# Kernel tuning notes

Hardware: AMD Instinct MI355X
Metric: run time of the kernel (lower is better)

## Reference

```python
import jax, jax.numpy as jnp
import numpy as np

IN_FEATURES = 1024
OUT_FEATURES = 1024
GRID_SIZE = 5
SPLINE_ORDER = 3
GRID_RANGE = (-1.0, 1.0)


def make_grid():
    h = (GRID_RANGE[1] - GRID_RANGE[0]) / GRID_SIZE
    g = jnp.arange(-SPLINE_ORDER, GRID_SIZE + SPLINE_ORDER + 1, dtype=jnp.float32) * h + GRID_RANGE[0]
    return jnp.tile(g[None, :], (IN_FEATURES, 1))  # (in, G + 2k + 1)


def b_splines(x, grid):
    # x: (N, in), grid: (in, G+2k+1) -> bases: (N, in, G+k)
    xe = x[..., None]
    bases = ((xe >= grid[:, :-1]) & (xe < grid[:, 1:])).astype(x.dtype)
    for k in range(1, SPLINE_ORDER + 1):
        left = (xe - grid[:, :-(k + 1)]) / (grid[:, k:-1] - grid[:, :-(k + 1)])
        right = (grid[:, k + 1:] - xe) / (grid[:, k + 1:] - grid[:, 1:-k])
        bases = left * bases[:, :, :-1] + right * bases[:, :, 1:]
    return bases


def setup_inputs() -> dict:
    key = jax.random.key(0)
    k1, k2, k3 = jax.random.split(key, 3)
    x = jax.random.uniform(k1, (8192, IN_FEATURES), dtype=jnp.float32)
    # lecun_normal-style init: std = 1/sqrt(fan_in)
    base_weight = jax.random.normal(k2, (OUT_FEATURES, IN_FEATURES), dtype=jnp.float32) / np.sqrt(IN_FEATURES)
    coeff = GRID_SIZE + SPLINE_ORDER
    spline_weight = jax.random.normal(k3, (OUT_FEATURES, IN_FEATURES, coeff), dtype=jnp.float32) / np.sqrt(IN_FEATURES * coeff)
    spline_scaler = jnp.ones((OUT_FEATURES, IN_FEATURES), dtype=jnp.float32)
    grid = make_grid()
    return {"x": x, "grid": grid, "base_weight": base_weight,
            "spline_weight": spline_weight, "spline_scaler": spline_scaler}


def reference(x, grid, base_weight, spline_weight, spline_scaler):
    N = x.shape[0]
    base_out = jax.nn.silu(x) @ base_weight.T  # (N, out)
    bases = b_splines(x, grid)                 # (N, in, G+k)
    scaled_sw = spline_weight * spline_scaler[..., None]  # (out, in, G+k)
    spline_out = bases.reshape(N, -1) @ scaled_sw.reshape(OUT_FEATURES, -1).T  # (N, out)
    return base_out + spline_out
```

## Files before the change

kernel.cpp:

```cpp
#include <hip/hip_runtime.h>
#include <hip/hip_bf16.h>

#define IN_F 1024
#define OUT_F 1024
#define KTOT (IN_F * 9)
#define M_ROWS 8192

#define BM 256
#define BN 128
#define BK 64
#define NT (KTOT / BK)

#define A_TILE_E 16384
#define B_TILE_E 8192

typedef short bf16x8 __attribute__((ext_vector_type(8)));
typedef int   i32x4  __attribute__((ext_vector_type(4)));
typedef float f32x4  __attribute__((ext_vector_type(4)));

#define AS1 __attribute__((address_space(1)))
#define AS3 __attribute__((address_space(3)))

__device__ __forceinline__ void kan_basis_fast(
    float xv, const float* __restrict__ g,
    const float* __restrict__ inv1, const float* __restrict__ inv2,
    const float* __restrict__ inv3, float* __restrict__ out) {
  float b[11];
#pragma unroll
  for (int j = 0; j < 11; ++j)
    b[j] = (xv >= g[j] && xv < g[j + 1]) ? 1.0f : 0.0f;
#pragma unroll
  for (int j = 0; j < 10; ++j)
    b[j] = (xv - g[j]) * inv1[j] * b[j] + (g[j + 2] - xv) * inv1[j + 1] * b[j + 1];
#pragma unroll
  for (int j = 0; j < 9; ++j)
    b[j] = (xv - g[j]) * inv2[j] * b[j] + (g[j + 3] - xv) * inv2[j + 1] * b[j + 1];
#pragma unroll
  for (int j = 0; j < 8; ++j)
    b[j] = (xv - g[j]) * inv3[j] * b[j] + (g[j + 4] - xv) * inv3[j + 1] * b[j + 1];
#pragma unroll
  for (int j = 0; j < 8; ++j) out[j] = b[j];
}

__global__ __launch_bounds__(256) void expand_a(
    const float* __restrict__ x, const float* __restrict__ grid,
    __hip_bfloat16* __restrict__ A, int row0, int nrows) {
  const int tid = threadIdx.x;
  const int lane = tid & 63;
  const int wvx = tid >> 6;
  const int l15 = lane & 15;
  const int lhi = lane >> 4;

  const int nb = blockIdx.x >> 3;
  const int ib = blockIdx.x & 7;
  const int n_l = nb * 16 + l15;
  const int i0 = ib * 128 + wvx * 32 + lhi * 8;

  const int bm = n_l >> 8, wm = (n_l >> 6) & 3, m = (n_l >> 4) & 3;

  float g[12];
  const float* gp = grid + (size_t)i0 * 12;
#pragma unroll
  for (int j = 0; j < 12; ++j) g[j] = gp[j];
  float inv1[11], inv2[10], inv3[9];
#pragma unroll
  for (int j = 0; j < 11; ++j) inv1[j] = 1.0f / (g[j + 1] - g[j]);
#pragma unroll
  for (int j = 0; j < 10; ++j) inv2[j] = 1.0f / (g[j + 2] - g[j]);
#pragma unroll
  for (int j = 0; j < 9; ++j)  inv3[j] = 1.0f / (g[j + 3] - g[j]);

  const float* xp = x + (size_t)(row0 + n_l) * IN_F + i0;
  float xs[8];
  *(f32x4*)&xs[0] = *(const f32x4*)xp;
  *(f32x4*)&xs[4] = *(const f32x4*)(xp + 4);

  bf16x8 out[9];
#pragma unroll
  for (int j = 0; j < 8; ++j) {
    float xv = xs[j];
    float bas[8];
    kan_basis_fast(xv, g, inv1, inv2, inv3, bas);
    float s = xv / (1.0f + __expf(-xv));
    out[0][j] = (short)__bfloat16_as_ushort(__float2bfloat16(s));
#pragma unroll
    for (int c = 0; c < 8; ++c)
      out[c + 1][j] = (short)__bfloat16_as_ushort(__float2bfloat16(bas[c]));
  }

#pragma unroll
  for (int c = 0; c < 9; ++c) {
    int k0 = c * IN_F + i0;
    int kt = k0 >> 6;
    int kk = (k0 >> 5) & 1;
    size_t frag = ((((size_t)bm * NT + kt) * 4 + wm) * 4 + m) * 2 + kk;
    *(bf16x8*)(A + frag * 512 + lane * 8) = out[c];
  }
}

__global__ __launch_bounds__(256) void pack_b(
    const float* __restrict__ bw, const float* __restrict__ sw,
    const float* __restrict__ sc, __hip_bfloat16* __restrict__ B) {
  const int tid = threadIdx.x;
  const int lane = tid & 63;
  const int wid = blockIdx.x * 4 + (tid >> 6);
  const int og = wid >> 5;
  const int ib32 = wid & 31;
  const int bn = og >> 3, colg = og & 7;
  const int l15 = lane & 15, lhi = lane >> 4;
  const int o = og * 16 + l15;
  const int i0 = ib32 * 32 + lhi * 8;

  float bwv[8], scv[8];
  const float* bp = bw + (size_t)o * IN_F + i0;
  const float* sp = sc + (size_t)o * IN_F + i0;
  *(f32x4*)&bwv[0] = *(const f32x4*)bp;
  *(f32x4*)&bwv[4] = *(const f32x4*)(bp + 4);
  *(f32x4*)&scv[0] = *(const f32x4*)sp;
  *(f32x4*)&scv[4] = *(const f32x4*)(sp + 4);

  bf16x8 out[9];
#pragma unroll
  for (int j = 0; j < 8; ++j) {
    out[0][j] = (short)__bfloat16_as_ushort(__float2bfloat16(bwv[j]));
    const float* swp = sw + ((size_t)o * IN_F + i0 + j) * 8;
    float swv[8];
    *(f32x4*)&swv[0] = *(const f32x4*)swp;
    *(f32x4*)&swv[4] = *(const f32x4*)(swp + 4);
#pragma unroll
    for (int c = 0; c < 8; ++c)
      out[c + 1][j] = (short)__bfloat16_as_ushort(__float2bfloat16(swv[c] * scv[j]));
  }

#pragma unroll
  for (int c = 0; c < 9; ++c) {
    int kt = c * 16 + (ib32 >> 1);
    int kk = ib32 & 1;
    size_t frag = ((size_t)bn * NT + kt) * 16 + colg * 2 + kk;
    *(bf16x8*)(B + frag * 512 + lane * 8) = out[c];
  }
}


__device__ __forceinline__ void gld16(const __hip_bfloat16* g, __hip_bfloat16* l) {
  __builtin_amdgcn_global_load_lds((AS1 void*)g, (AS3 void*)l, 16, 0, 0);
}

__device__ __forceinline__ bf16x8 dsr128(uint32_t addr) {
  i32x4 r;
  asm volatile("ds_read_b128 %0, %1" : "=v"(r) : "v"(addr));
  return __builtin_bit_cast(bf16x8, r);
}

#define SB __builtin_amdgcn_sched_barrier(0)

#define SLOT_B 49152
#define SLOT_E 24576

#define READ_FRAGS(dA, dB, slot, h) do {                                   \
    uint32_t s_ = ldsB + (uint32_t)(slot) * SLOT_B;                        \
    _Pragma("unroll")                                                      \
    for (int m_ = 0; m_ < 4; ++m_) dA[m_] = dsr128(s_ + aOff[h][m_]);      \
    _Pragma("unroll")                                                      \
    for (int n_ = 0; n_ < 4; ++n_) dB[n_] = dsr128(s_ + bOff[h][n_]);      \
  } while (0)

#define MFMA_BURST(sA, sB) do {                                            \
    __builtin_amdgcn_s_setprio(1);                                         \
    _Pragma("unroll")                                                      \
    for (int m_ = 0; m_ < 4; ++m_)                                         \
      _Pragma("unroll")                                                    \
      for (int n_ = 0; n_ < 4; ++n_)                                       \
        acc[m_][n_] = __builtin_amdgcn_mfma_f32_16x16x32_bf16(             \
            sA[m_], sB[n_], acc[m_][n_], 0, 0, 0);                         \
    __builtin_amdgcn_s_setprio(0);                                         \
  } while (0)

#define STAGE_T(slot, t) do {                                              \
    __hip_bfloat16* d_ = ldsP + (slot) * SLOT_E;                           \
    const __hip_bfloat16* aT_ = aG + (size_t)(t) * A_TILE_E;               \
    const __hip_bfloat16* bT_ = bG + (size_t)(t) * B_TILE_E;               \
    gld16(aT_,         d_ + dstE);                                         \
    gld16(aT_ + 4096,  d_ + dstE + 4096);                                  \
    gld16(aT_ + 8192,  d_ + dstE + 8192);                                  \
    gld16(aT_ + 12288, d_ + dstE + 12288);                                 \
    gld16(bT_,         d_ + 16384 + dstE);                                 \
    gld16(bT_ + 4096,  d_ + 16384 + dstE + 4096);                          \
  } while (0)

#define TILE_FULL(t) do {                                                  \
    const int nxt_ = cur == 2 ? 0 : cur + 1;                               \
    const int stg_ = cur == 0 ? 2 : cur - 1;                               \
    READ_FRAGS(ga, gb, cur, 1);                               \
    STAGE_T(stg_, (t) + 2);                                  \
    SB;                                                                    \
    asm volatile("s_waitcnt lgkmcnt(8)" ::: "memory"); SB;                 \
    MFMA_BURST(fa, fb);                                                    \
    SB;                                                                    \
    asm volatile("s_waitcnt lgkmcnt(0)" ::: "memory"); SB;                 \
    asm volatile("s_waitcnt vmcnt(6)" ::: "memory"); SB;                   \
    __builtin_amdgcn_s_barrier(); SB;                     \
    READ_FRAGS(fa, fb, nxt_, 0);                               \
    SB;                                                                    \
    MFMA_BURST(ga, gb);                                                    \
    SB;                                                                    \
    cur = nxt_;                                                            \
  } while (0)

#define TILE_NT2() do {                                                    \
    const int nxt_ = cur == 2 ? 0 : cur + 1;                               \
    READ_FRAGS(ga, gb, cur, 1);                                            \
    SB;                                                                    \
    asm volatile("s_waitcnt lgkmcnt(8)" ::: "memory"); SB;                 \
    MFMA_BURST(fa, fb);                                                    \
    SB;                                                                    \
    asm volatile("s_waitcnt lgkmcnt(0)" ::: "memory"); SB;                 \
    asm volatile("s_waitcnt vmcnt(0)" ::: "memory"); SB;                   \
    __builtin_amdgcn_s_barrier(); SB;                                      \
    READ_FRAGS(fa, fb, nxt_, 0);                                           \
    SB;                                                                    \
    MFMA_BURST(ga, gb);                                                    \
    SB;                                                                    \
    cur = nxt_;                                                            \
  } while (0)

#define TILE_LAST() do {                                                   \
    READ_FRAGS(ga, gb, cur, 1);                                            \
    SB;                                                                    \
    asm volatile("s_waitcnt lgkmcnt(8)" ::: "memory"); SB;                 \
    MFMA_BURST(fa, fb);                                                    \
    SB;                                                                    \
    asm volatile("s_waitcnt lgkmcnt(0)" ::: "memory"); SB;                 \
    MFMA_BURST(ga, gb);                                                    \
    SB;                                                                    \
  } while (0)

__global__ __launch_bounds__(512, 2) void gemm_v11(
    const __hip_bfloat16* __restrict__ A, const __hip_bfloat16* __restrict__ B,
    float* __restrict__ C) {
  __shared__ __align__(16) __hip_bfloat16 S[3][SLOT_E];

  const int nwg = gridDim.x;
  const int q = nwg >> 3;
  const int L = (blockIdx.x & 7) * q + (blockIdx.x >> 3);
  const int bm = L >> 3, bn = L & 7;

  const int tid = threadIdx.x;
  const int lane = tid & 63;
  const int wv = tid >> 6;
  const int wm = wv >> 1;
  const int wn = wv & 1;
  const int l15 = lane & 15, lhi = lane >> 4;

  const __hip_bfloat16* aG = A + (size_t)bm * NT * A_TILE_E + (wv * 64 + lane) * 8;
  const __hip_bfloat16* bG = B + (size_t)bn * NT * B_TILE_E + (wv * 64 + lane) * 8;
  __hip_bfloat16* ldsP = &S[0][0];
  const int dstE = wv * 512;

  const uint32_t ldsB = (uint32_t)(uintptr_t)(AS3 const void*)&S[0][0];
  uint32_t aOff[2][4], bOff[2][4];
#pragma unroll
  for (int h = 0; h < 2; ++h)
#pragma unroll
    for (int m = 0; m < 4; ++m) {
      aOff[h][m] = (uint32_t)((wm * 8 + m * 2 + h) * 1024 + lane * 16);
      bOff[h][m] = (uint32_t)(32768 + ((wn * 4 + m) * 2 + h) * 1024 + lane * 16);
    }

  f32x4 acc[4][4];
#pragma unroll
  for (int m = 0; m < 4; ++m)
#pragma unroll
    for (int n = 0; n < 4; ++n) acc[m][n] = f32x4{0.f, 0.f, 0.f, 0.f};

  bf16x8 fa[4], fb[4];
  bf16x8 ga[4], gb[4];

  STAGE_T(0, 0);
  STAGE_T(1, 1);
  asm volatile("s_waitcnt vmcnt(6)" ::: "memory");
  SB;
  __builtin_amdgcn_s_barrier();
  SB;
  READ_FRAGS(fa, fb, 0, 0);
  SB;

  int cur = 0;
  for (int t = 0; t < NT - 2; ++t) TILE_FULL(t);
  TILE_NT2();
  TILE_LAST();

#pragma unroll
  for (int m = 0; m < 4; ++m)
#pragma unroll
    for (int n = 0; n < 4; ++n) {
      int col = bn * BN + wn * 64 + n * 16 + l15;
      int row0 = bm * BM + wm * 64 + m * 16 + lhi * 4;
#pragma unroll
      for (int j = 0; j < 4; ++j)
        C[(size_t)(row0 + j) * OUT_F + col] = acc[m][n][j];
    }
}

__global__ __launch_bounds__(256) void kan_naive(
    const float* __restrict__ x, const float* __restrict__ grid,
    const float* __restrict__ bw, const float* __restrict__ sw,
    const float* __restrict__ sc, float* __restrict__ out) {
  __shared__ float s_act[IN_F];
  __shared__ float s_bas[IN_F * 8];
  int n = blockIdx.x;
  for (int i = threadIdx.x; i < IN_F; i += 256) {
    float xv = x[(size_t)n * IN_F + i];
    float g[12];
    const float* gp = grid + i * 12;
#pragma unroll
    for (int t = 0; t < 12; ++t) g[t] = gp[t];
    float b[11];
#pragma unroll
    for (int j = 0; j < 11; ++j)
      b[j] = (xv >= g[j] && xv < g[j + 1]) ? 1.0f : 0.0f;
#pragma unroll
    for (int k = 1; k <= 3; ++k)
#pragma unroll
      for (int j = 0; j < 11 - k; ++j) {
        float left = (xv - g[j]) / (g[j + k] - g[j]);
        float right = (g[j + k + 1] - xv) / (g[j + k + 1] - g[j + 1]);
        b[j] = left * b[j] + right * b[j + 1];
      }
    s_act[i] = xv / (1.0f + __expf(-xv));
#pragma unroll
    for (int c = 0; c < 8; ++c) s_bas[i * 8 + c] = b[c];
  }
  __syncthreads();
  for (int o = threadIdx.x; o < OUT_F; o += 256) {
    float acc = 0.f;
    const float* bwo = bw + (size_t)o * IN_F;
    const float* swo = sw + (size_t)o * IN_F * 8;
    const float* sco = sc + (size_t)o * IN_F;
    for (int i = 0; i < IN_F; ++i) {
      acc += s_act[i] * bwo[i];
      float p = 0.f;
#pragma unroll
      for (int c = 0; c < 8; ++c) p += s_bas[i * 8 + c] * swo[i * 8 + c];
      acc += p * sco[i];
    }
    out[(size_t)n * OUT_F + o] = acc;
  }
}

extern "C" void kernel_launch(void* const* d_in, const int* in_sizes, int n_in,
                              void* d_out, int out_size, void* d_ws, size_t ws_size,
                              hipStream_t stream) {
  const float* x  = (const float*)d_in[0];
  const float* grid = (const float*)d_in[1];
  const float* bw = (const float*)d_in[2];
  const float* sw = (const float*)d_in[3];
  const float* sc = (const float*)d_in[4];
  float* out = (float*)d_out;

  const size_t Bbytes = (size_t)OUT_F * KTOT * 2;
  const size_t rowBytes = (size_t)KTOT * 2;

  if (ws_size >= Bbytes + 256 * rowBytes) {
    __hip_bfloat16* Bp = (__hip_bfloat16*)d_ws;
    __hip_bfloat16* Ap = (__hip_bfloat16*)((char*)d_ws + Bbytes);
    size_t arows = (ws_size - Bbytes) / rowBytes;
    int chunk = (int)((arows / 256) * 256);
    if (chunk > M_ROWS) chunk = M_ROWS;

    pack_b<<<OUT_F * 128 / 256, 256, 0, stream>>>(bw, sw, sc, Bp);
    for (int r0 = 0; r0 < M_ROWS; r0 += chunk) {
      int rows = M_ROWS - r0 < chunk ? M_ROWS - r0 : chunk;
      expand_a<<<(rows / 16) * 8, 256, 0, stream>>>(x, grid, Ap, r0, rows);
      gemm_v11<<<(rows / BM) * 8, 512, 0, stream>>>(Ap, Bp, out + (size_t)r0 * OUT_F);
    }
  } else {
    kan_naive<<<M_ROWS, 256, 0, stream>>>(x, grid, bw, sw, sc, out);
  }
}
```

Baseline: 183.4 us.

## Use 256x256 tiles with split-K halves and atomic accumulation in GEMM

Enlarges each workgroup's output tile from 256x128 to 256x256 and splits the K dimension into two halves across workgroups, with results summed via atomicAdd into a zero-initialised output. Staging moves from a triple buffer to a double buffer, and LDS reads now use immediate offsets, which cuts address arithmetic. The aim is higher arithmetic intensity per loaded byte while keeping the same workgroup count. The cost is an extra memset, atomic traffic on the output, nondeterministic summation order, and higher register pressure from 32 accumulators per wave.

```diff
diff --git a/kernel.cpp b/kernel.cpp
--- a/kernel.cpp
+++ b/kernel.cpp
@@ -6,10 +6,9 @@
 #define KTOT (IN_F * 9)
 #define M_ROWS 8192
 
-#define BM 256
-#define BN 128
 #define BK 64
 #define NT (KTOT / BK)
+#define NT_H (NT / 2)
 
 #define A_TILE_E 16384
 #define B_TILE_E 8192
@@ -106,7 +105,7 @@
   const int wid = blockIdx.x * 4 + (tid >> 6);
   const int og = wid >> 5;
   const int ib32 = wid & 31;
-  const int bn = og >> 3, colg = og & 7;
+  const int obn = og >> 3, colg = og & 7;
   const int l15 = lane & 15, lhi = lane >> 4;
   const int o = og * 16 + l15;
   const int i0 = ib32 * 32 + lhi * 8;
@@ -136,7 +135,7 @@
   for (int c = 0; c < 9; ++c) {
     int kt = c * 16 + (ib32 >> 1);
     int kk = ib32 & 1;
-    size_t frag = ((size_t)bn * NT + kt) * 16 + colg * 2 + kk;
+    size_t frag = ((size_t)obn * NT + kt) * 16 + colg * 2 + kk;
     *(bf16x8*)(B + frag * 512 + lane * 8) = out[c];
   }
 }
@@ -146,29 +145,39 @@
   __builtin_amdgcn_global_load_lds((AS1 void*)g, (AS3 void*)l, 16, 0, 0);
 }
 
-__device__ __forceinline__ bf16x8 dsr128(uint32_t addr) {
-  i32x4 r;
-  asm volatile("ds_read_b128 %0, %1" : "=v"(r) : "v"(addr));
-  return __builtin_bit_cast(bf16x8, r);
-}
+#define DSRO(dst, addr, IMM)                                               \
+  asm volatile("ds_read_b128 %0, %1 offset:" #IMM : "=v"(dst) : "v"(addr))
 
 #define SB __builtin_amdgcn_sched_barrier(0)
 
-#define SLOT_B 49152
-#define SLOT_E 24576
-
-#define READ_FRAGS(dA, dB, slot, h) do {                                   \
-    uint32_t s_ = ldsB + (uint32_t)(slot) * SLOT_B;                        \
-    _Pragma("unroll")                                                      \
-    for (int m_ = 0; m_ < 4; ++m_) dA[m_] = dsr128(s_ + aOff[h][m_]);      \
-    _Pragma("unroll")                                                      \
-    for (int n_ = 0; n_ < 4; ++n_) dB[n_] = dsr128(s_ + bOff[h][n_]);      \
-  } while (0)
-
-#define MFMA_BURST(sA, sB) do {                                            \
+#define SLOT_E 32768
+#define SLOT_B 65536
+
+#define READ_A_KK0(d, aA) do {                                             \
+    DSRO(d[0], aA, 0);     DSRO(d[1], aA, 2048);                           \
+    DSRO(d[2], aA, 4096);  DSRO(d[3], aA, 6144);                           \
+    DSRO(d[4], aA, 8192);  DSRO(d[5], aA, 10240);                          \
+    DSRO(d[6], aA, 12288); DSRO(d[7], aA, 14336);                          \
+  } while (0)
+#define READ_A_KK1(d, aA) do {                                             \
+    DSRO(d[0], aA, 1024);  DSRO(d[1], aA, 3072);                           \
+    DSRO(d[2], aA, 5120);  DSRO(d[3], aA, 7168);                           \
+    DSRO(d[4], aA, 9216);  DSRO(d[5], aA, 11264);                          \
+    DSRO(d[6], aA, 13312); DSRO(d[7], aA, 15360);                          \
+  } while (0)
+#define READ_B_KK0(d, bA) do {                                             \
+    DSRO(d[0], bA, 0);     DSRO(d[1], bA, 2048);                           \
+    DSRO(d[2], bA, 4096);  DSRO(d[3], bA, 6144);                           \
+  } while (0)
+#define READ_B_KK1(d, bA) do {                                             \
+    DSRO(d[0], bA, 1024);  DSRO(d[1], bA, 3072);                           \
+    DSRO(d[2], bA, 5120);  DSRO(d[3], bA, 7168);                           \
+  } while (0)
+
+#define MFMA_B(sA, sB) do {                                                \
     __builtin_amdgcn_s_setprio(1);                                         \
     _Pragma("unroll")                                                      \
-    for (int m_ = 0; m_ < 4; ++m_)                                         \
+    for (int m_ = 0; m_ < 8; ++m_)                                         \
       _Pragma("unroll")                                                    \
       for (int n_ = 0; n_ < 4; ++n_)                                       \
         acc[m_][n_] = __builtin_amdgcn_mfma_f32_16x16x32_bf16(             \
@@ -176,129 +185,105 @@
     __builtin_amdgcn_s_setprio(0);                                         \
   } while (0)
 
-#define STAGE_T(slot, t) do {                                              \
-    __hip_bfloat16* d_ = ldsP + (slot) * SLOT_E;                           \
-    const __hip_bfloat16* aT_ = aG + (size_t)(t) * A_TILE_E;               \
-    const __hip_bfloat16* bT_ = bG + (size_t)(t) * B_TILE_E;               \
-    gld16(aT_,         d_ + dstE);                                         \
-    gld16(aT_ + 4096,  d_ + dstE + 4096);                                  \
-    gld16(aT_ + 8192,  d_ + dstE + 8192);                                  \
-    gld16(aT_ + 12288, d_ + dstE + 12288);                                 \
-    gld16(bT_,         d_ + 16384 + dstE);                                 \
-    gld16(bT_ + 4096,  d_ + 16384 + dstE + 4096);                          \
-  } while (0)
-
-#define TILE_FULL(t) do {                                                  \
-    const int nxt_ = cur == 2 ? 0 : cur + 1;                               \
-    const int stg_ = cur == 0 ? 2 : cur - 1;                               \
-    READ_FRAGS(ga, gb, cur, 1);                               \
-    STAGE_T(stg_, (t) + 2);                                  \
+#define STAGE12(DST) do {                                                  \
+    gld16(aGp,          (DST) + dstE);                                     \
+    gld16(aGp + 4096,   (DST) + dstE + 4096);                              \
+    gld16(aGp + 8192,   (DST) + dstE + 8192);                              \
+    gld16(aGp + 12288,  (DST) + dstE + 12288);                             \
+    gld16(bGp0,         (DST) + dstE + 16384);                             \
+    gld16(bGp0 + 4096,  (DST) + dstE + 20480);                             \
+    gld16(bGp1,         (DST) + dstE + 24576);                             \
+    gld16(bGp1 + 4096,  (DST) + dstE + 28672);                             \
+    aGp += 16384; bGp0 += 8192; bGp1 += 8192;                              \
+  } while (0)
+
+#define TILE_V12(cA, cB, nA, nB, STAGE_, READN_) do {                      \
+    READ_A_KK1(ga, cA); READ_B_KK1(gb, cB);                   \
+    STAGE_                                                                 \
     SB;                                                                    \
-    asm volatile("s_waitcnt lgkmcnt(8)" ::: "memory"); SB;                 \
-    MFMA_BURST(fa, fb);                                                    \
-    SB;                                                                    \
-    asm volatile("s_waitcnt lgkmcnt(0)" ::: "memory"); SB;                 \
-    asm volatile("s_waitcnt vmcnt(6)" ::: "memory"); SB;                   \
-    __builtin_amdgcn_s_barrier(); SB;                     \
-    READ_FRAGS(fa, fb, nxt_, 0);                               \
-    SB;                                                                    \
-    MFMA_BURST(ga, gb);                                                    \
-    SB;                                                                    \
-    cur = nxt_;                                                            \
-  } while (0)
-
-#define TILE_NT2() do {                                                    \
-    const int nxt_ = cur == 2 ? 0 : cur + 1;                               \
-    READ_FRAGS(ga, gb, cur, 1);                                            \
-    SB;                                                                    \
-    asm volatile("s_waitcnt lgkmcnt(8)" ::: "memory"); SB;                 \
-    MFMA_BURST(fa, fb);                                                    \
+    asm volatile("s_waitcnt lgkmcnt(12)" ::: "memory"); SB;                \
+    MFMA_B(fa, fb);                                                        \
     SB;                                                                    \
     asm volatile("s_waitcnt lgkmcnt(0)" ::: "memory"); SB;                 \
     asm volatile("s_waitcnt vmcnt(0)" ::: "memory"); SB;                   \
-    __builtin_amdgcn_s_barrier(); SB;                                      \
-    READ_FRAGS(fa, fb, nxt_, 0);                                           \
+    __builtin_amdgcn_s_barrier(); SB;               \
+    READN_                                                                 \
     SB;                                                                    \
-    MFMA_BURST(ga, gb);                                                    \
+    MFMA_B(ga, gb);                                                        \
     SB;                                                                    \
-    cur = nxt_;                                                            \
-  } while (0)
-
-#define TILE_LAST() do {                                                   \
-    READ_FRAGS(ga, gb, cur, 1);                                            \
-    SB;                                                                    \
-    asm volatile("s_waitcnt lgkmcnt(8)" ::: "memory"); SB;                 \
-    MFMA_BURST(fa, fb);                                                    \
-    SB;                                                                    \
-    asm volatile("s_waitcnt lgkmcnt(0)" ::: "memory"); SB;                 \
-    MFMA_BURST(ga, gb);                                                    \
-    SB;                                                                    \
-  } while (0)
-
-__global__ __launch_bounds__(512, 2) void gemm_v11(
+  } while (0)
+
+#define READN12(nA, nB) READ_A_KK0(fa, nA); READ_B_KK0(fb, nB);
+
+__global__ __launch_bounds__(512, 2) void gemm_v12(
     const __hip_bfloat16* __restrict__ A, const __hip_bfloat16* __restrict__ B,
     float* __restrict__ C) {
-  __shared__ __align__(16) __hip_bfloat16 S[3][SLOT_E];
+  __shared__ __align__(16) __hip_bfloat16 S[2][SLOT_E];
 
   const int nwg = gridDim.x;
   const int q = nwg >> 3;
   const int L = (blockIdx.x & 7) * q + (blockIdx.x >> 3);
-  const int bm = L >> 3, bn = L & 7;
+  const int bm = L >> 3;
+  const int khalf = (L >> 2) & 1;
+  const int bn2 = L & 3;
 
   const int tid = threadIdx.x;
   const int lane = tid & 63;
   const int wv = tid >> 6;
-  const int wm = wv >> 1;
-  const int wn = wv & 1;
+  const int wm = wv >> 2;
+  const int wn = wv & 3;
   const int l15 = lane & 15, lhi = lane >> 4;
 
-  const __hip_bfloat16* aG = A + (size_t)bm * NT * A_TILE_E + (wv * 64 + lane) * 8;
-  const __hip_bfloat16* bG = B + (size_t)bn * NT * B_TILE_E + (wv * 64 + lane) * 8;
+  const int laneE = (wv * 64 + lane) * 8;
+  const __hip_bfloat16* aGp =
+      A + ((size_t)bm * NT + khalf * NT_H) * A_TILE_E + laneE;
+  const __hip_bfloat16* bGp0 =
+      B + ((size_t)(2 * bn2) * NT + khalf * NT_H) * B_TILE_E + laneE;
+  const __hip_bfloat16* bGp1 =
+      B + ((size_t)(2 * bn2 + 1) * NT + khalf * NT_H) * B_TILE_E + laneE;
   __hip_bfloat16* ldsP = &S[0][0];
   const int dstE = wv * 512;
 
   const uint32_t ldsB = (uint32_t)(uintptr_t)(AS3 const void*)&S[0][0];
-  uint32_t aOff[2][4], bOff[2][4];
-#pragma unroll
-  for (int h = 0; h < 2; ++h)
-#pragma unroll
-    for (int m = 0; m < 4; ++m) {
-      aOff[h][m] = (uint32_t)((wm * 8 + m * 2 + h) * 1024 + lane * 16);
-      bOff[h][m] = (uint32_t)(32768 + ((wn * 4 + m) * 2 + h) * 1024 + lane * 16);
-    }
-
-  f32x4 acc[4][4];
-#pragma unroll
-  for (int m = 0; m < 4; ++m)
+  const uint32_t aA0 = ldsB + wm * 16384 + lane * 16;
+  const uint32_t aA1 = aA0 + SLOT_B;
+  const uint32_t bA0 = ldsB + 32768 + (wn >> 1) * 16384 + (wn & 1) * 8192 + lane * 16;
+  const uint32_t bA1 = bA0 + SLOT_B;
+
+  f32x4 acc[8][4];
+#pragma unroll
+  for (int m = 0; m < 8; ++m)
 #pragma unroll
     for (int n = 0; n < 4; ++n) acc[m][n] = f32x4{0.f, 0.f, 0.f, 0.f};
 
-  bf16x8 fa[4], fb[4];
-  bf16x8 ga[4], gb[4];
-
-  STAGE_T(0, 0);
-  STAGE_T(1, 1);
-  asm volatile("s_waitcnt vmcnt(6)" ::: "memory");
+  bf16x8 fa[8], fb[4];
+  bf16x8 ga[8], gb[4];
+
+  STAGE12(ldsP);
+  asm volatile("s_waitcnt vmcnt(0)" ::: "memory");
   SB;
   __builtin_amdgcn_s_barrier();
   SB;
-  READ_FRAGS(fa, fb, 0, 0);
+  READ_A_KK0(fa, aA0); READ_B_KK0(fb, bA0);
   SB;
 
-  int cur = 0;
-  for (int t = 0; t < NT - 2; ++t) TILE_FULL(t);
-  TILE_NT2();
-  TILE_LAST();
-
-#pragma unroll
-  for (int m = 0; m < 4; ++m)
+#pragma unroll 1
+  for (int tt = 0; tt < (NT_H - 2) / 2; ++tt) {
+    TILE_V12(aA0, bA0, aA1, bA1, STAGE12(ldsP + SLOT_E);, READN12(aA1, bA1));
+    TILE_V12(aA1, bA1, aA0, bA0, STAGE12(ldsP);,          READN12(aA0, bA0));
+  }
+  TILE_V12(aA0, bA0, aA1, bA1, STAGE12(ldsP + SLOT_E);, READN12(aA1, bA1));
+  TILE_V12(aA1, bA1, aA0, bA0, ;, ;);
+
+#pragma unroll
+  for (int m = 0; m < 8; ++m)
 #pragma unroll
     for (int n = 0; n < 4; ++n) {
-      int col = bn * BN + wn * 64 + n * 16 + l15;
-      int row0 = bm * BM + wm * 64 + m * 16 + lhi * 4;
+      int col = bn2 * 256 + (wn >> 1) * 128 + (wn & 1) * 64 + n * 16 + l15;
+      int row0 = bm * 256 + wm * 128 + m * 16 + lhi * 4;
 #pragma unroll
       for (int j = 0; j < 4; ++j)
-        C[(size_t)(row0 + j) * OUT_F + col] = acc[m][n][j];
+        atomicAdd(&C[(size_t)(row0 + j) * OUT_F + col], acc[m][n][j]);
     }
 }
 
@@ -368,11 +353,12 @@
     int chunk = (int)((arows / 256) * 256);
     if (chunk > M_ROWS) chunk = M_ROWS;
 
+    hipMemsetAsync(d_out, 0, (size_t)out_size * sizeof(float), stream);
     pack_b<<<OUT_F * 128 / 256, 256, 0, stream>>>(bw, sw, sc, Bp);
     for (int r0 = 0; r0 < M_ROWS; r0 += chunk) {
       int rows = M_ROWS - r0 < chunk ? M_ROWS - r0 : chunk;
       expand_a<<<(rows / 16) * 8, 256, 0, stream>>>(x, grid, Ap, r0, rows);
-      gemm_v11<<<(rows / BM) * 8, 512, 0, stream>>>(Ap, Bp, out + (size_t)r0 * OUT_F);
+      gemm_v12<<<(rows / 256) * 8, 512, 0, stream>>>(Ap, Bp, out + (size_t)r0 * OUT_F);
     }
   } else {
     kan_naive<<<M_ROWS, 256, 0, stream>>>(x, grid, bw, sw, sc, out);
```

Result: slower. 217.4 us (+18.5%).
